# Kernel tuning notes

Measured on AMD Instinct MI355X. Metric: run time of the kernel, lower is better.

Reference implementation:

```python
import jax, jax.numpy as jnp
import numpy as np

NUM_SEGMENTS = 65536  # matches fill_max of index; torch_scatter uses index.max()+1


def setup_inputs() -> dict:
    key = jax.random.key(0)
    k1, k2 = jax.random.split(key)
    N, D = 4194304, 64
    x = jax.random.normal(k1, (N, D), dtype=jnp.float32)
    index = jnp.sort(jax.random.randint(k2, (N,), 0, NUM_SEGMENTS, dtype=jnp.int64))
    return {"x": x, "index": index}


def reference(x, index):
    # scatter_max along dim 0: out[s, d] = max over i with index[i]==s of x[i, d]
    seg_max = jax.ops.segment_max(x, index, num_segments=NUM_SEGMENTS)
    # torch_scatter initializes the output with zeros, so empty segments yield 0
    return jnp.where(jnp.isneginf(seg_max), jnp.zeros_like(seg_max), seg_max)
```

## Files before the change

kernel.cpp:

```cpp
#include <hip/hip_runtime.h>
#include <stdint.h>
#include <math.h>

#define NSEG 65536
#define D 64

__global__ __launch_bounds__(256) void seg_bounds_kernel(const int* __restrict__ index,
                                                         int N, int* __restrict__ start) {
    const int s = blockIdx.x * 256 + threadIdx.x;
    if (s > NSEG) return;
    int lo = 0, hi = N;
    while (lo < hi) {
        const int mid = (lo + hi) >> 1;
        if (index[mid] < s) lo = mid + 1; else hi = mid;
    }
    start[s] = lo;
}

__global__ __launch_bounds__(256) void segmax_kernel(const float* __restrict__ x,
                                                     const int* __restrict__ start,
                                                     float* __restrict__ out) {
    const int lane = threadIdx.x & 63;
    const int wave = threadIdx.x >> 6;
    const int s = blockIdx.x * 4 + wave;

    const int rs = start[s];
    const int re = start[s + 1];

    const int sub  = lane >> 4;
    const int col4 = (lane & 15) * 4;

    float4 m;
    if (rs < re) {
        m = make_float4(-INFINITY, -INFINITY, -INFINITY, -INFINITY);
        for (int r0 = rs; r0 < re; r0 += 4) {
            int r = r0 + sub;
            if (r >= re) r = re - 1;
            const float4 v = *reinterpret_cast<const float4*>(x + (size_t)r * D + col4);
            m.x = fmaxf(m.x, v.x);
            m.y = fmaxf(m.y, v.y);
            m.z = fmaxf(m.z, v.z);
            m.w = fmaxf(m.w, v.w);
        }
        m.x = fmaxf(m.x, __shfl_xor(m.x, 16));
        m.y = fmaxf(m.y, __shfl_xor(m.y, 16));
        m.z = fmaxf(m.z, __shfl_xor(m.z, 16));
        m.w = fmaxf(m.w, __shfl_xor(m.w, 16));
        m.x = fmaxf(m.x, __shfl_xor(m.x, 32));
        m.y = fmaxf(m.y, __shfl_xor(m.y, 32));
        m.z = fmaxf(m.z, __shfl_xor(m.z, 32));
        m.w = fmaxf(m.w, __shfl_xor(m.w, 32));
    } else {
        m = make_float4(0.0f, 0.0f, 0.0f, 0.0f);
    }

    if (lane < 16) {
        *reinterpret_cast<float4*>(out + (size_t)s * D + col4) = m;
    }
}

extern "C" void kernel_launch(void* const* d_in, const int* in_sizes, int n_in,
                              void* d_out, int out_size, void* d_ws, size_t ws_size,
                              hipStream_t stream) {
    const float* x   = (const float*)d_in[0];
    const int* index = (const int*)d_in[1];
    float* out       = (float*)d_out;
    int* start       = (int*)d_ws;

    const int N = in_sizes[0] / D;

    seg_bounds_kernel<<<(NSEG + 1 + 255) / 256, 256, 0, stream>>>(index, N, start);
    segmax_kernel<<<NSEG / 4, 256, 0, stream>>>(x, start, out);
}
```

Before: 209.8 us.

## Replace binary-search segment bounds with linear scan and unroll nontemporal segmax loads

Segment start offsets are now computed with a parallel linear scan over the sorted index, where each thread handles 16 entries and writes a boundary whenever the value changes. This replaces the per-segment binary search with its dependent random global reads. The segmax loop is unrolled by two with separate accumulators, uses nontemporal loads, and handles the tail without clamped duplicate loads. The scan assumes N is a multiple of 16 and that the index buffer is 16-byte aligned.

```diff
diff --git a/kernel.cpp b/kernel.cpp
--- a/kernel.cpp
+++ b/kernel.cpp
@@ -5,16 +5,34 @@
 #define NSEG 65536
 #define D 64
 
-__global__ __launch_bounds__(256) void seg_bounds_kernel(const int* __restrict__ index,
-                                                         int N, int* __restrict__ start) {
-    const int s = blockIdx.x * 256 + threadIdx.x;
-    if (s > NSEG) return;
-    int lo = 0, hi = N;
-    while (lo < hi) {
-        const int mid = (lo + hi) >> 1;
-        if (index[mid] < s) lo = mid + 1; else hi = mid;
+typedef float f32x4 __attribute__((ext_vector_type(4)));
+
+__global__ __launch_bounds__(256) void seg_bounds_scan(const int* __restrict__ index,
+                                                       int N, int* __restrict__ start) {
+    const int t  = blockIdx.x * 256 + threadIdx.x;
+    const int i0 = t * 16;
+    if (i0 >= N) return;
+
+    int prev = (i0 == 0) ? -1 : index[i0 - 1];
+
+    int4 a0 = reinterpret_cast<const int4*>(index + i0)[0];
+    int4 a1 = reinterpret_cast<const int4*>(index + i0)[1];
+    int4 a2 = reinterpret_cast<const int4*>(index + i0)[2];
+    int4 a3 = reinterpret_cast<const int4*>(index + i0)[3];
+    int v[16] = {a0.x, a0.y, a0.z, a0.w, a1.x, a1.y, a1.z, a1.w,
+                 a2.x, a2.y, a2.z, a2.w, a3.x, a3.y, a3.z, a3.w};
+
+#pragma unroll
+    for (int j = 0; j < 16; ++j) {
+        const int cur = v[j];
+        if (cur != prev) {
+            for (int s = prev + 1; s <= cur; ++s) start[s] = i0 + j;
+            prev = cur;
+        }
     }
-    start[s] = lo;
+    if (i0 + 16 >= N) {
+        for (int s = prev + 1; s <= NSEG; ++s) start[s] = N;
+    }
 }
 
 __global__ __launch_bounds__(256) void segmax_kernel(const float* __restrict__ x,
@@ -30,18 +48,37 @@
     const int sub  = lane >> 4;
     const int col4 = (lane & 15) * 4;
 
-    float4 m;
+    f32x4 m;
     if (rs < re) {
-        m = make_float4(-INFINITY, -INFINITY, -INFINITY, -INFINITY);
-        for (int r0 = rs; r0 < re; r0 += 4) {
-            int r = r0 + sub;
-            if (r >= re) r = re - 1;
-            const float4 v = *reinterpret_cast<const float4*>(x + (size_t)r * D + col4);
-            m.x = fmaxf(m.x, v.x);
-            m.y = fmaxf(m.y, v.y);
-            m.z = fmaxf(m.z, v.z);
-            m.w = fmaxf(m.w, v.w);
+        f32x4 m0 = {-INFINITY, -INFINITY, -INFINITY, -INFINITY};
+        f32x4 m1 = m0;
+        int r0 = rs;
+        for (; r0 + 8 <= re; r0 += 8) {
+            const f32x4 v0 = __builtin_nontemporal_load(
+                reinterpret_cast<const f32x4*>(x + (size_t)(r0 + sub) * D + col4));
+            const f32x4 v1 = __builtin_nontemporal_load(
+                reinterpret_cast<const f32x4*>(x + (size_t)(r0 + 4 + sub) * D + col4));
+            m0.x = fmaxf(m0.x, v0.x); m0.y = fmaxf(m0.y, v0.y);
+            m0.z = fmaxf(m0.z, v0.z); m0.w = fmaxf(m0.w, v0.w);
+            m1.x = fmaxf(m1.x, v1.x); m1.y = fmaxf(m1.y, v1.y);
+            m1.z = fmaxf(m1.z, v1.z); m1.w = fmaxf(m1.w, v1.w);
         }
+        if (r0 + 4 <= re) {
+            const f32x4 v = __builtin_nontemporal_load(
+                reinterpret_cast<const f32x4*>(x + (size_t)(r0 + sub) * D + col4));
+            m0.x = fmaxf(m0.x, v.x); m0.y = fmaxf(m0.y, v.y);
+            m0.z = fmaxf(m0.z, v.z); m0.w = fmaxf(m0.w, v.w);
+            r0 += 4;
+        }
+        const int r = r0 + sub;
+        if (r < re) {
+            const f32x4 v = __builtin_nontemporal_load(
+                reinterpret_cast<const f32x4*>(x + (size_t)r * D + col4));
+            m1.x = fmaxf(m1.x, v.x); m1.y = fmaxf(m1.y, v.y);
+            m1.z = fmaxf(m1.z, v.z); m1.w = fmaxf(m1.w, v.w);
+        }
+        m.x = fmaxf(m0.x, m1.x); m.y = fmaxf(m0.y, m1.y);
+        m.z = fmaxf(m0.z, m1.z); m.w = fmaxf(m0.w, m1.w);
         m.x = fmaxf(m.x, __shfl_xor(m.x, 16));
         m.y = fmaxf(m.y, __shfl_xor(m.y, 16));
         m.z = fmaxf(m.z, __shfl_xor(m.z, 16));
@@ -51,11 +88,11 @@
         m.z = fmaxf(m.z, __shfl_xor(m.z, 32));
         m.w = fmaxf(m.w, __shfl_xor(m.w, 32));
     } else {
-        m = make_float4(0.0f, 0.0f, 0.0f, 0.0f);
+        m = (f32x4){0.0f, 0.0f, 0.0f, 0.0f};
     }
 
     if (lane < 16) {
-        *reinterpret_cast<float4*>(out + (size_t)s * D + col4) = m;
+        *reinterpret_cast<f32x4*>(out + (size_t)s * D + col4) = m;
     }
 }
 
@@ -69,6 +106,6 @@
 
     const int N = in_sizes[0] / D;
 
-    seg_bounds_kernel<<<(NSEG + 1 + 255) / 256, 256, 0, stream>>>(index, N, start);
+    seg_bounds_scan<<<(N / 16 + 255) / 256, 256, 0, stream>>>(index, N, start);
     segmax_kernel<<<NSEG / 4, 256, 0, stream>>>(x, start, out);
 }
```

After: 187.6 us. 10.6% less time.
